# Optimization experiments

Hardware: AMD Instinct MI355X
Metric: run time of the kernel (lower is better)

The kernel has to match this reference:

```python
import jax, jax.numpy as jnp
import numpy as np

HEAD_DIM = 128
NUM_HEADS = 16
GROUP_SIZE = 8


def setup_inputs() -> dict:
    key = jax.random.key(0)
    k1, k2, k3 = jax.random.split(key, 3)
    B, T, K = 2, 2048, 2048
    query = jax.random.normal(k1, (B, T, NUM_HEADS * HEAD_DIM), dtype=jnp.float32)
    k_ = jax.random.normal(k2, (B, K, NUM_HEADS, HEAD_DIM), dtype=jnp.float32)
    v_ = jax.random.normal(k3, (B, K, NUM_HEADS, HEAD_DIM), dtype=jnp.float32)
    return {"query": query, "key": k_, "value": v_}


def reference(query, key, value):
    B, T, _ = query.shape
    g = GROUP_SIZE
    # (B, T//g, g, H, D)
    gq = query.reshape(B, T // g, g, NUM_HEADS, HEAD_DIM)
    scale = jnp.sqrt(jnp.asarray(HEAD_DIM, dtype=query.dtype))
    # scores: (B, T//g, g, H, K)
    scores = jnp.einsum('btghd,bkhd->btghk', gq, key) / scale
    attention = jax.nn.softmax(scores, axis=-1)
    out = jnp.einsum('btghk,bkhd->btghd', attention, value)
    return out.reshape(B, T, -1)
```

## Files before the change

kernel.cpp:

```cpp
#include <hip/hip_runtime.h>


#define T_   2048
#define KLEN 2048
#define H_   16
#define D_   128
#define BH_  32
#define NT_  (KLEN / 64)

typedef unsigned short u16;
typedef short bf16x8 __attribute__((ext_vector_type(8), may_alias));
typedef float f32x4 __attribute__((ext_vector_type(4)));
typedef float f32x8 __attribute__((ext_vector_type(8), may_alias));
typedef float f32x16 __attribute__((ext_vector_type(16)));
typedef unsigned int u32a __attribute__((may_alias));
typedef u16 u16a __attribute__((may_alias));

__device__ __forceinline__ u16 f2bf(float f) {
    unsigned int u = __builtin_bit_cast(unsigned int, f);
    u += 0x7fffu + ((u >> 16) & 1u);
    return (u16)(u >> 16);
}
__device__ __forceinline__ unsigned int pk2(float a, float b) {
    unsigned int r;
    asm("v_cvt_pk_bf16_f32 %0, %1, %2" : "=v"(r) : "v"(a), "v"(b));
    return r;
}
__device__ __forceinline__ void pl_swap(unsigned int& a, unsigned int& b) {
    asm("v_permlane32_swap_b32 %0, %1" : "+v"(a), "+v"(b));
}

__device__ __forceinline__ void async_cp16(const void* g, void* l) {
    __builtin_amdgcn_global_load_lds(
        (const __attribute__((address_space(1))) unsigned int*)g,
        (__attribute__((address_space(3))) unsigned int*)l, 16, 0, 0);
}

#define FR_ELEMS ((size_t)KLEN * D_)
#define WS_NEED  (2 * BH_ * FR_ELEMS * sizeof(u16))
#define SM_BUF   32768

__global__ __launch_bounds__(256)
void prep_fused(const float* __restrict__ k_g, const float* __restrict__ v_g,
                u16* __restrict__ kf, u16* __restrict__ vf) {
    __shared__ __align__(16) unsigned char smk[16384];
    __shared__ __align__(16) unsigned char smv[16384];
    const int kt64 = blockIdx.x & 31;
    const int bh   = blockIdx.x >> 5;
    const int b = bh >> 4, h = bh & 15;
    const int tid = threadIdx.x;

    {
        const float* kbase = k_g + ((size_t)(b * KLEN + kt64 * 64) * H_ + h) * D_;
        #pragma unroll
        for (int i = 0; i < 4; ++i) {
            const int gid  = tid + 256 * i;
            const int row  = gid >> 4;
            const int col8 = gid & 15;
            f32x8 kv = *(const f32x8*)(kbase + (size_t)row * (H_ * D_) + col8 * 8);
            uint4 w;
            w.x = pk2(kv[0], kv[1]); w.y = pk2(kv[2], kv[3]);
            w.z = pk2(kv[4], kv[5]); w.w = pk2(kv[6], kv[7]);
            *(uint4*)(smk + row * 256 + ((col8 ^ (row & 15)) * 16)) = w;
        }
    }
    {
        const float* vbase = v_g + ((size_t)b * KLEN * H_ + h) * D_;
        const int sc0 = tid & 15;
        const int spr = tid >> 4;
        #pragma unroll
        for (int rr = 0; rr < 2; ++rr) {
            const int r0 = 2 * (spr + 16 * rr);
            const float* vp = vbase + (size_t)(kt64 * 64 + r0) * (H_ * D_) + sc0 * 8;
            f32x8 va = *(const f32x8*)vp;
            f32x8 vb = *(const f32x8*)(vp + H_ * D_);
            const int g_hi = r0 >> 3;
            const int woff = (r0 & 7) * 2;
            #pragma unroll
            for (int j = 0; j < 8; ++j) {
                const int d = sc0 * 8 + j;
                const int g = g_hi ^ ((d ^ (d >> 3)) & 7);
                *(u32a*)(smv + d * 128 + g * 16 + woff) = pk2(va[j], vb[j]);
            }
        }
    }
    __syncthreads();
    {
        u16* obase = kf + (size_t)bh * FR_ELEMS + (size_t)kt64 * 8192;
        #pragma unroll
        for (int i = 0; i < 4; ++i) {
            const int gid    = tid + 256 * i;
            const int lane   = gid & 63;
            const int dchunk = (gid >> 6) & 7;
            const int ktile  = gid >> 9;
            const int key  = ktile * 32 + (lane & 31);
            const int col8 = dchunk * 2 + (lane >> 5);
            uint4 w = *(const uint4*)(smk + key * 256 + ((col8 ^ (key & 15)) * 16));
            *(uint4*)(obase + (size_t)gid * 8) = w;
        }
    }
    {
        u16* obase = vf + (size_t)bh * FR_ELEMS;
        #pragma unroll
        for (int i = 0; i < 4; ++i) {
            const int gid   = tid + 256 * i;
            const int lane  = gid & 63;
            const int ntile = (gid >> 6) & 3;
            const int kc    = (gid >> 8) & 3;
            const int key0  = kc * 16 + (lane >> 5) * 8;
            const int d     = ntile * 32 + (lane & 31);
            const int g     = (key0 >> 3) ^ ((d ^ (d >> 3)) & 7);
            uint4 w = *(const uint4*)(smv + d * 128 + g * 16);
            *(uint4*)(obase + ((size_t)(kt64 * 16 + kc * 4 + ntile) * 64 + lane) * 8) = w;
        }
    }
}


struct PA2 { bf16x8 f0, f1; };

__device__ __forceinline__ PA2 softmax_pack(f32x16 st, float kexp, float& lacc) {
    float p[16];
    #pragma unroll
    for (int r = 0; r < 16; ++r) p[r] = exp2f(st[r] * kexp);
    lacc += (((p[0] + p[1]) + (p[2] + p[3])) + ((p[4] + p[5]) + (p[6] + p[7])))
          + (((p[8] + p[9]) + (p[10] + p[11])) + ((p[12] + p[13]) + (p[14] + p[15])));
    unsigned int a0 = pk2(p[0], p[1]),   b0 = pk2(p[4], p[5]);
    unsigned int a1 = pk2(p[2], p[3]),   b1 = pk2(p[6], p[7]);
    unsigned int a2 = pk2(p[8], p[9]),   b2 = pk2(p[12], p[13]);
    unsigned int a3 = pk2(p[10], p[11]), b3 = pk2(p[14], p[15]);
    pl_swap(a0, b0); pl_swap(a1, b1); pl_swap(a2, b2); pl_swap(a3, b3);
    uint4 w0; w0.x = a0; w0.y = a1; w0.z = b0; w0.w = b1;
    uint4 w1; w1.x = a2; w1.y = a3; w1.z = b2; w1.w = b3;
    PA2 r;
    r.f0 = __builtin_bit_cast(bf16x8, w0);
    r.f1 = __builtin_bit_cast(bf16x8, w1);
    return r;
}

__global__ __launch_bounds__(256, 2)
void gqa_fa6(const float* __restrict__ q_g, const u16* __restrict__ kf,
             const u16* __restrict__ vf, float* __restrict__ o_g) {
    __shared__ __align__(16) unsigned char smem[2 * SM_BUF];

    const int lane = threadIdx.x & 63;
    const int wave = threadIdx.x >> 6;
    const int half = lane >> 5;
    const int col  = lane & 31;

    const int blk = blockIdx.x;
    const int bh  = (blk & 7) * 4 + (blk >> 7);
    const int qt  = (blk >> 3) & 15;
    const int b = bh >> 4, h = bh & 15;

    const int q0 = qt * 128 + wave * 32;

    bf16x8 qf[8];
    {
        const float* qbase = q_g + (size_t)(b * T_ + q0 + col) * (H_ * D_)
                                 + h * D_ + half * 8;
        #pragma unroll
        for (int dchunk = 0; dchunk < 8; ++dchunk) {
            f32x8 qv = *(const f32x8*)(qbase + dchunk * 16);
            uint4 w;
            w.x = pk2(qv[0], qv[1]); w.y = pk2(qv[2], qv[3]);
            w.z = pk2(qv[4], qv[5]); w.w = pk2(qv[6], qv[7]);
            qf[dchunk] = __builtin_bit_cast(bf16x8, w);
        }
    }

    const u16* KFb = kf + (size_t)bh * FR_ELEMS;
    const u16* VFb = vf + (size_t)bh * FR_ELEMS;

    f32x16 acc[4] = {};
    float l_part = 0.f;

    const float kexp = 0.12751744f;

    auto stage = [&](int buf, int kt) {
        const u16* ksrc = KFb + (size_t)kt * 8192;
        const u16* vsrc = VFb + (size_t)kt * 8192;
        unsigned char* base = smem + buf * SM_BUF;
        #pragma unroll
        for (int j = 0; j < 8; ++j) {
            const int idx = wave * 8 + j;
            if (idx < 16)
                async_cp16(ksrc + idx * 512 + lane * 8, base + idx * 1024);
            else
                async_cp16(vsrc + (idx - 16) * 512 + lane * 8,
                           base + 16384 + (idx - 16) * 1024);
        }
    };

    stage(0, 0);
    __syncthreads();

    for (int kt = 0; kt < NT_; ++kt) {
        const int cur = kt & 1;
        if (kt + 1 < NT_) stage(cur ^ 1, kt + 1);

        const unsigned char* kbuf = smem + cur * SM_BUF;
        const unsigned char* vbuf = kbuf + 16384;

        f32x16 s0 = {}, s1 = {};
        __builtin_amdgcn_s_setprio(1);
        #pragma unroll
        for (int dchunk = 0; dchunk < 8; ++dchunk) {
            bf16x8 kfr0 = *(const bf16x8*)(kbuf + dchunk * 1024 + lane * 16);
            bf16x8 kfr1 = *(const bf16x8*)(kbuf + (8 + dchunk) * 1024 + lane * 16);
            s0 = __builtin_amdgcn_mfma_f32_32x32x16_bf16(kfr0, qf[dchunk], s0, 0, 0, 0);
            s1 = __builtin_amdgcn_mfma_f32_32x32x16_bf16(kfr1, qf[dchunk], s1, 0, 0, 0);
        }
        __builtin_amdgcn_s_setprio(0);

        PA2 pa01 = softmax_pack(s0, kexp, l_part);
        PA2 pa23 = softmax_pack(s1, kexp, l_part);

        bf16x8 pfrag0 = pa01.f0, pfrag1 = pa01.f1;
        bf16x8 pfrag2 = pa23.f0, pfrag3 = pa23.f1;
        __builtin_amdgcn_s_setprio(1);
        #pragma unroll
        for (int kc = 0; kc < 4; ++kc) {
            const bf16x8 paf = (kc == 0) ? pfrag0 : (kc == 1) ? pfrag1
                             : (kc == 2) ? pfrag2 : pfrag3;
            #pragma unroll
            for (int nt2 = 0; nt2 < 4; ++nt2) {
                bf16x8 vfr = *(const bf16x8*)(vbuf + (kc * 4 + nt2) * 1024 + lane * 16);
                acc[nt2] = __builtin_amdgcn_mfma_f32_32x32x16_bf16(paf, vfr, acc[nt2], 0, 0, 0);
            }
        }
        __builtin_amdgcn_s_setprio(0);

        __syncthreads();
    }

    const float l_full = l_part + __shfl_xor(l_part, 32);
    float* lds_l = (float*)smem;
    if (half == 0) lds_l[wave * 32 + col] = 1.f / l_full;
    __syncthreads();
    #pragma unroll
    for (int r = 0; r < 16; ++r) {
        const int qrow = (r & 3) + 8 * (r >> 2) + 4 * half;
        const float inv = lds_l[wave * 32 + qrow];
        float* op = o_g + (size_t)(b * T_ + q0 + qrow) * (H_ * D_) + h * D_ + col;
        #pragma unroll
        for (int nt2 = 0; nt2 < 4; ++nt2)
            op[nt2 * 32] = acc[nt2][r] * inv;
    }
}


#define VT_BYTES 16384
#define KT_BYTES (64 * 136 * 2)
#define PWF_BYTES 2304

__global__ __launch_bounds__(256, 2)
void gqa_fa_v1(const float* __restrict__ q_g, const float* __restrict__ k_g,
               const float* __restrict__ v_g, float* __restrict__ o_g) {
    __shared__ __align__(16) unsigned char smem[VT_BYTES + KT_BYTES + 4 * PWF_BYTES];
    unsigned char* VtB = smem;
    unsigned char* KtB = smem + VT_BYTES;
    const int lane = threadIdx.x & 63;
    const int wave = threadIdx.x >> 6;
    const int c    = lane & 15;
    const int quad = lane >> 4;
    const int qt = blockIdx.x & 31;
    const int bh = blockIdx.x >> 5;
    const int h  = bh & 15;
    const int b  = bh >> 4;
    const int q0 = qt * 64 + wave * 16;
    bf16x8 qf[4];
    {
        const float* qbase = q_g + (size_t)(b * T_ + q0 + c) * (H_ * D_) + h * D_ + quad * 8;
        #pragma unroll
        for (int dc = 0; dc < 4; ++dc) {
            f32x8 qv = *(const f32x8*)(qbase + dc * 32);
            uint4 w;
            w.x = pk2(qv[0], qv[1]); w.y = pk2(qv[2], qv[3]);
            w.z = pk2(qv[4], qv[5]); w.w = pk2(qv[6], qv[7]);
            qf[dc] = __builtin_bit_cast(bf16x8, w);
        }
    }
    f32x4 acc_o[8];
    #pragma unroll
    for (int dt = 0; dt < 8; ++dt) acc_o[dt] = (f32x4){0.f, 0.f, 0.f, 0.f};
    float m_i[4], l_i[4];
    #pragma unroll
    for (int r = 0; r < 4; ++r) { m_i[r] = -1e30f; l_i[r] = 0.f; }
    const float kexp = 0.12751744f;
    unsigned char* Pw = smem + VT_BYTES + KT_BYTES + wave * PWF_BYTES;
    const int sc0 = threadIdx.x & 15;
    const int spr = threadIdx.x >> 4;
    const size_t kvstride = (size_t)(H_ * D_);
    const float* kbase = k_g + ((size_t)b * KLEN * H_ + h) * D_;
    const float* vbase = v_g + ((size_t)b * KLEN * H_ + h) * D_;
    for (int kt = 0; kt < KLEN / 64; ++kt) {
        __syncthreads();
        #pragma unroll
        for (int i = 0; i < 4; ++i) {
            const int id   = threadIdx.x + 256 * i;
            const int row  = id >> 4;
            const int dcol = (id & 15) * 8;
            const float* kp = kbase + (size_t)(kt * 64 + row) * kvstride + dcol;
            f32x8 kv = *(const f32x8*)kp;
            uint4 w;
            w.x = pk2(kv[0], kv[1]); w.y = pk2(kv[2], kv[3]);
            w.z = pk2(kv[4], kv[5]); w.w = pk2(kv[6], kv[7]);
            *(uint4*)(KtB + (row * 136 + dcol) * 2) = w;
        }
        #pragma unroll
        for (int rr = 0; rr < 2; ++rr) {
            const int r0 = 2 * (spr + 16 * rr);
            const float* vp = vbase + (size_t)(kt * 64 + r0) * kvstride + sc0 * 8;
            f32x8 va = *(const f32x8*)vp;
            f32x8 vb = *(const f32x8*)(vp + kvstride);
            const int g_hi = r0 >> 3;
            const int woff = (r0 & 7) * 2;
            #pragma unroll
            for (int j = 0; j < 8; ++j) {
                const int d = sc0 * 8 + j;
                const int g = g_hi ^ ((d ^ (d >> 3)) & 7);
                *(u32a*)(VtB + d * 128 + g * 16 + woff) = pk2(va[j], vb[j]);
            }
        }
        __syncthreads();
        f32x4 s[4];
        #pragma unroll
        for (int nt = 0; nt < 4; ++nt) {
            s[nt] = (f32x4){0.f, 0.f, 0.f, 0.f};
            const u16* kfp = (const u16*)KtB + (nt * 16 + c) * 136 + quad * 8;
            #pragma unroll
            for (int dc = 0; dc < 4; ++dc) {
                bf16x8 kfr = *(const bf16x8*)(kfp + dc * 32);
                s[nt] = __builtin_amdgcn_mfma_f32_16x16x32_bf16(qf[dc], kfr, s[nt], 0, 0, 0);
            }
        }
        #pragma unroll
        for (int r = 0; r < 4; ++r) {
            float v = fmaxf(fmaxf(s[0][r], s[1][r]), fmaxf(s[2][r], s[3][r]));
            v = fmaxf(v, __shfl_xor(v, 1));
            v = fmaxf(v, __shfl_xor(v, 2));
            v = fmaxf(v, __shfl_xor(v, 4));
            v = fmaxf(v, __shfl_xor(v, 8));
            const float mnew  = fmaxf(m_i[r], v);
            const float alpha = exp2f((m_i[r] - mnew) * kexp);
            m_i[r] = mnew;
            l_i[r] *= alpha;
            #pragma unroll
            for (int dt = 0; dt < 8; ++dt) acc_o[dt][r] *= alpha;
            float sum = 0.f;
            #pragma unroll
            for (int nt = 0; nt < 4; ++nt) {
                const float p = exp2f((s[nt][r] - mnew) * kexp);
                sum += p;
                *(u16a*)(Pw + ((quad * 4 + r) * 72 + nt * 16 + c) * 2) = f2bf(p);
            }
            float t = sum;
            t += __shfl_xor(t, 1);
            t += __shfl_xor(t, 2);
            t += __shfl_xor(t, 4);
            t += __shfl_xor(t, 8);
            l_i[r] += t;
        }
        __syncthreads();
        #pragma unroll
        for (int kc = 0; kc < 2; ++kc) {
            bf16x8 pf = *(const bf16x8*)(Pw + (c * 72 + kc * 32 + quad * 8) * 2);
            const int k0 = kc * 32 + quad * 8;
            #pragma unroll
            for (int dt = 0; dt < 8; ++dt) {
                const int d = dt * 16 + c;
                const int g = (k0 >> 3) ^ ((d ^ (d >> 3)) & 7);
                bf16x8 vfr = *(const bf16x8*)(VtB + d * 128 + g * 16);
                acc_o[dt] = __builtin_amdgcn_mfma_f32_16x16x32_bf16(pf, vfr, acc_o[dt], 0, 0, 0);
            }
        }
    }
    #pragma unroll
    for (int r = 0; r < 4; ++r) {
        const float inv = 1.f / l_i[r];
        const int qrow = q0 + quad * 4 + r;
        float* op = o_g + (size_t)(b * T_ + qrow) * (H_ * D_) + h * D_ + c;
        #pragma unroll
        for (int dt = 0; dt < 8; ++dt)
            op[dt * 16] = acc_o[dt][r] * inv;
    }
}

extern "C" void kernel_launch(void* const* d_in, const int* in_sizes, int n_in,
                              void* d_out, int out_size, void* d_ws, size_t ws_size,
                              hipStream_t stream) {
    const float* q = (const float*)d_in[0];
    const float* k = (const float*)d_in[1];
    const float* v = (const float*)d_in[2];
    float* o = (float*)d_out;
    if (ws_size >= WS_NEED) {
        u16* kfb = (u16*)d_ws;
        u16* vfb = kfb + (size_t)BH_ * FR_ELEMS;
        prep_fused<<<dim3(1024), dim3(256), 0, stream>>>(k, v, kfb, vfb);
        gqa_fa6<<<dim3(512), dim3(256), 0, stream>>>(q, kfb, vfb, o);
    } else {
        gqa_fa_v1<<<dim3(1024), dim3(256), 0, stream>>>(q, k, v, o);
    }
}
```

Before: 211.5 us.

## Process two 32-row query tiles per wave to reuse K/V fragments

Each wave now handles 64 query rows (two 32-row tiles) instead of 32, so each K and V fragment read from LDS feeds two MFMAs. The grid halves to 256 blocks of 256 rows each, and launch bounds drop to one block per CU to leave room for the doubled accumulators and Q fragments. This aims to cut LDS traffic and K/V staging per unit of work. The cost is fewer waves in flight for latency hiding and only 256 blocks on a 256-CU part, so occupancy falls.

```diff
diff --git a/kernel.cpp b/kernel.cpp
--- a/kernel.cpp
+++ b/kernel.cpp
@@ -138,8 +138,8 @@
     return r;
 }
 
-__global__ __launch_bounds__(256, 2)
-void gqa_fa6(const float* __restrict__ q_g, const u16* __restrict__ kf,
+__global__ __launch_bounds__(256, 1)
+void gqa_fa7(const float* __restrict__ q_g, const u16* __restrict__ kf,
              const u16* __restrict__ vf, float* __restrict__ o_g) {
     __shared__ __align__(16) unsigned char smem[2 * SM_BUF];
 
@@ -149,13 +149,13 @@
     const int col  = lane & 31;
 
     const int blk = blockIdx.x;
-    const int bh  = (blk & 7) * 4 + (blk >> 7);
-    const int qt  = (blk >> 3) & 15;
+    const int bh  = (blk & 7) * 4 + (blk >> 6);
+    const int qt  = (blk >> 3) & 7;
     const int b = bh >> 4, h = bh & 15;
 
-    const int q0 = qt * 128 + wave * 32;
-
-    bf16x8 qf[8];
+    const int q0 = qt * 256 + wave * 64;
+
+    bf16x8 qfA[8], qfB[8];
     {
         const float* qbase = q_g + (size_t)(b * T_ + q0 + col) * (H_ * D_)
                                  + h * D_ + half * 8;
@@ -165,15 +165,24 @@
             uint4 w;
             w.x = pk2(qv[0], qv[1]); w.y = pk2(qv[2], qv[3]);
             w.z = pk2(qv[4], qv[5]); w.w = pk2(qv[6], qv[7]);
-            qf[dchunk] = __builtin_bit_cast(bf16x8, w);
+            qfA[dchunk] = __builtin_bit_cast(bf16x8, w);
+        }
+        const float* qbase2 = qbase + (size_t)32 * (H_ * D_);
+        #pragma unroll
+        for (int dchunk = 0; dchunk < 8; ++dchunk) {
+            f32x8 qv = *(const f32x8*)(qbase2 + dchunk * 16);
+            uint4 w;
+            w.x = pk2(qv[0], qv[1]); w.y = pk2(qv[2], qv[3]);
+            w.z = pk2(qv[4], qv[5]); w.w = pk2(qv[6], qv[7]);
+            qfB[dchunk] = __builtin_bit_cast(bf16x8, w);
         }
     }
 
     const u16* KFb = kf + (size_t)bh * FR_ELEMS;
     const u16* VFb = vf + (size_t)bh * FR_ELEMS;
 
-    f32x16 acc[4] = {};
-    float l_part = 0.f;
+    f32x16 accA[4] = {}, accB[4] = {};
+    float l_A = 0.f, l_B = 0.f;
 
     const float kexp = 0.12751744f;
 
@@ -202,31 +211,36 @@
         const unsigned char* kbuf = smem + cur * SM_BUF;
         const unsigned char* vbuf = kbuf + 16384;
 
-        f32x16 s0 = {}, s1 = {};
+        f32x16 sA0 = {}, sA1 = {}, sB0 = {}, sB1 = {};
         __builtin_amdgcn_s_setprio(1);
         #pragma unroll
         for (int dchunk = 0; dchunk < 8; ++dchunk) {
             bf16x8 kfr0 = *(const bf16x8*)(kbuf + dchunk * 1024 + lane * 16);
             bf16x8 kfr1 = *(const bf16x8*)(kbuf + (8 + dchunk) * 1024 + lane * 16);
-            s0 = __builtin_amdgcn_mfma_f32_32x32x16_bf16(kfr0, qf[dchunk], s0, 0, 0, 0);
-            s1 = __builtin_amdgcn_mfma_f32_32x32x16_bf16(kfr1, qf[dchunk], s1, 0, 0, 0);
+            sA0 = __builtin_amdgcn_mfma_f32_32x32x16_bf16(kfr0, qfA[dchunk], sA0, 0, 0, 0);
+            sA1 = __builtin_amdgcn_mfma_f32_32x32x16_bf16(kfr1, qfA[dchunk], sA1, 0, 0, 0);
+            sB0 = __builtin_amdgcn_mfma_f32_32x32x16_bf16(kfr0, qfB[dchunk], sB0, 0, 0, 0);
+            sB1 = __builtin_amdgcn_mfma_f32_32x32x16_bf16(kfr1, qfB[dchunk], sB1, 0, 0, 0);
         }
         __builtin_amdgcn_s_setprio(0);
 
-        PA2 pa01 = softmax_pack(s0, kexp, l_part);
-        PA2 pa23 = softmax_pack(s1, kexp, l_part);
-
-        bf16x8 pfrag0 = pa01.f0, pfrag1 = pa01.f1;
-        bf16x8 pfrag2 = pa23.f0, pfrag3 = pa23.f1;
+        PA2 pA01 = softmax_pack(sA0, kexp, l_A);
+        PA2 pA23 = softmax_pack(sA1, kexp, l_A);
+        PA2 pB01 = softmax_pack(sB0, kexp, l_B);
+        PA2 pB23 = softmax_pack(sB1, kexp, l_B);
+
         __builtin_amdgcn_s_setprio(1);
         #pragma unroll
         for (int kc = 0; kc < 4; ++kc) {
-            const bf16x8 paf = (kc == 0) ? pfrag0 : (kc == 1) ? pfrag1
-                             : (kc == 2) ? pfrag2 : pfrag3;
+            const bf16x8 pa = (kc == 0) ? pA01.f0 : (kc == 1) ? pA01.f1
+                            : (kc == 2) ? pA23.f0 : pA23.f1;
+            const bf16x8 pb = (kc == 0) ? pB01.f0 : (kc == 1) ? pB01.f1
+                            : (kc == 2) ? pB23.f0 : pB23.f1;
             #pragma unroll
             for (int nt2 = 0; nt2 < 4; ++nt2) {
                 bf16x8 vfr = *(const bf16x8*)(vbuf + (kc * 4 + nt2) * 1024 + lane * 16);
-                acc[nt2] = __builtin_amdgcn_mfma_f32_32x32x16_bf16(paf, vfr, acc[nt2], 0, 0, 0);
+                accA[nt2] = __builtin_amdgcn_mfma_f32_32x32x16_bf16(pa, vfr, accA[nt2], 0, 0, 0);
+                accB[nt2] = __builtin_amdgcn_mfma_f32_32x32x16_bf16(pb, vfr, accB[nt2], 0, 0, 0);
             }
         }
         __builtin_amdgcn_s_setprio(0);
@@ -234,18 +248,26 @@
         __syncthreads();
     }
 
-    const float l_full = l_part + __shfl_xor(l_part, 32);
+    const float lA_full = l_A + __shfl_xor(l_A, 32);
+    const float lB_full = l_B + __shfl_xor(l_B, 32);
     float* lds_l = (float*)smem;
-    if (half == 0) lds_l[wave * 32 + col] = 1.f / l_full;
+    if (half == 0) {
+        lds_l[wave * 64 + col]      = 1.f / lA_full;
+        lds_l[wave * 64 + 32 + col] = 1.f / lB_full;
+    }
     __syncthreads();
     #pragma unroll
     for (int r = 0; r < 16; ++r) {
         const int qrow = (r & 3) + 8 * (r >> 2) + 4 * half;
-        const float inv = lds_l[wave * 32 + qrow];
-        float* op = o_g + (size_t)(b * T_ + q0 + qrow) * (H_ * D_) + h * D_ + col;
-        #pragma unroll
-        for (int nt2 = 0; nt2 < 4; ++nt2)
-            op[nt2 * 32] = acc[nt2][r] * inv;
+        const float invA = lds_l[wave * 64 + qrow];
+        const float invB = lds_l[wave * 64 + 32 + qrow];
+        float* opA = o_g + (size_t)(b * T_ + q0 + qrow) * (H_ * D_) + h * D_ + col;
+        float* opB = opA + (size_t)32 * (H_ * D_);
+        #pragma unroll
+        for (int nt2 = 0; nt2 < 4; ++nt2) {
+            opA[nt2 * 32] = accA[nt2][r] * invA;
+            opB[nt2 * 32] = accB[nt2][r] * invB;
+        }
     }
 }
 
@@ -398,7 +420,7 @@
         u16* kfb = (u16*)d_ws;
         u16* vfb = kfb + (size_t)BH_ * FR_ELEMS;
         prep_fused<<<dim3(1024), dim3(256), 0, stream>>>(k, v, kfb, vfb);
-        gqa_fa6<<<dim3(512), dim3(256), 0, stream>>>(q, kfb, vfb, o);
+        gqa_fa7<<<dim3(256), dim3(256), 0, stream>>>(q, kfb, vfb, o);
     } else {
         gqa_fa_v1<<<dim3(1024), dim3(256), 0, stream>>>(q, k, v, o);
     }
```

Result: slower. 237.9 us (+12.5%).
